# Performance work log

Measured on AMD Instinct MI355X. Metric: run time of the kernel, lower is better.

The kernel has to match this reference:

```python
import jax, jax.numpy as jnp
import numpy as np

B, C, N, K, L = 4, 256, 8192, 4, 3


def _mlp2(h, W1, b1, W2, b2):
    return jax.nn.relu(h @ W1 + b1) @ W2 + b2


def setup_inputs() -> dict:
    key = jax.random.key(0)
    ks = jax.random.split(key, 12)
    s = lambda fan_in: 1.0 / np.sqrt(fan_in)
    inp = {
        "x": jax.random.normal(ks[0], (B, C, N), jnp.float32),
        "points": jax.random.normal(ks[1], (N, 3), jnp.float32),
        "neighbors": jax.random.randint(ks[2], (N, K), 0, N, jnp.int32),
        "edge_W1": jax.random.normal(ks[3], (3, C // 4), jnp.float32) * s(3),
        "edge_b1": jnp.zeros((C // 4,), jnp.float32),
        "edge_W2": jax.random.normal(ks[4], (C // 4, C // 2), jnp.float32) * s(C // 4),
        "edge_b2": jnp.zeros((C // 2,), jnp.float32),
        "msg_W1": jax.random.normal(ks[5], (L, 2 * C + C // 2, 2 * C), jnp.float32) * s(2 * C + C // 2),
        "msg_b1": jnp.zeros((L, 2 * C), jnp.float32),
        "msg_W2": jax.random.normal(ks[6], (L, 2 * C, C), jnp.float32) * s(2 * C),
        "msg_b2": jnp.zeros((L, C), jnp.float32),
        "upd_W1": jax.random.normal(ks[7], (L, 2 * C, 2 * C), jnp.float32) * s(2 * C),
        "upd_b1": jnp.zeros((L, 2 * C), jnp.float32),
        "upd_W2": jax.random.normal(ks[8], (L, 2 * C, C), jnp.float32) * s(2 * C),
        "upd_b2": jnp.zeros((L, C), jnp.float32),
    }
    return inp


def reference(x, points, neighbors, edge_W1, edge_b1, edge_W2, edge_b2,
              msg_W1, msg_b1, msg_W2, msg_b2, upd_W1, upd_b1, upd_W2, upd_b2):
    # x: [B, C, N] -> features [B, N, C]
    feats = jnp.transpose(x, (0, 2, 1))
    # edge features shared across layers: [N, K, C//2]
    edge_vec = points[neighbors] - points[:, None, :]          # [N, K, 3]
    edge_feat = _mlp2(edge_vec, edge_W1, edge_b1, edge_W2, edge_b2)
    for l in range(L):
        sender = feats[:, neighbors, :]                         # [B, N, K, C]
        receiver = jnp.broadcast_to(feats[:, :, None, :], sender.shape)
        ef = jnp.broadcast_to(edge_feat[None], (feats.shape[0],) + edge_feat.shape)
        msg_in = jnp.concatenate([sender, receiver, ef], axis=-1)  # [B,N,K,2.5C]
        msg = _mlp2(msg_in, msg_W1[l], msg_b1[l], msg_W2[l], msg_b2[l])
        agg = jnp.mean(msg, axis=2)                             # [B, N, C]
        upd_in = jnp.concatenate([feats, agg], axis=-1)         # [B, N, 2C]
        feats = _mlp2(upd_in, upd_W1[l], upd_b1[l], upd_W2[l], upd_b2[l])
    return jnp.transpose(feats, (0, 2, 1))
```

## Files before the change

kernel.cpp:

```cpp
#include <hip/hip_runtime.h>

#define DEVI __device__ __forceinline__

typedef unsigned short u16;
typedef unsigned int   u32;
typedef __attribute__((ext_vector_type(8))) short short8;
typedef __attribute__((ext_vector_type(4))) short short4b;
typedef __attribute__((ext_vector_type(4))) float f32x4;

DEVI float bf2f(u16 u) {
    union { u32 i; float f; } x; x.i = ((u32)u) << 16; return x.f;
}
DEVI u16 f2bf(float f) {
    u32 u = __float_as_uint(f);
    u32 r = (u + 0x7FFFu + ((u >> 16) & 1u)) >> 16;
    return (u16)r;
}

DEVI void gload_lds16(const void* g, void* l) {
    __builtin_amdgcn_global_load_lds((const __attribute__((address_space(1))) void*)g,
                                     (__attribute__((address_space(3))) void*)l, 16, 0, 0);
}

struct PJob { u32 dst, soff, tbase, ld, Kd, src; };
__device__ const PJob g_jobs[19] = {
    {0,        0,      0,    128, 64,  4},
    {8192,     0,      8,    512, 256, 0},
    {139264,   131072, 136,  512, 256, 0},
    {270336,   262144, 264,  512, 128, 0},
    {335872,   0,      328,  256, 512, 1},
    {466944,   0,      456,  512, 512, 2},
    {729088,   0,      712,  256, 512, 3},
    {860160,   327680, 840,  512, 256, 0},
    {991232,   458752, 968,  512, 256, 0},
    {1122304,  589824, 1096, 512, 128, 0},
    {1187840,  131072, 1160, 256, 512, 1},
    {1318912,  262144, 1288, 512, 512, 2},
    {1581056,  131072, 1544, 256, 512, 3},
    {1712128,  655360, 1672, 512, 256, 0},
    {1843200,  786432, 1800, 512, 256, 0},
    {1974272,  917504, 1928, 512, 128, 0},
    {2039808,  262144, 1992, 256, 512, 1},
    {2170880,  524288, 2120, 512, 512, 2},
    {2433024,  262144, 2376, 256, 512, 3},
};

__global__ void prep_weights(const float* __restrict__ mW1, const float* __restrict__ mW2,
                             const float* __restrict__ uW1, const float* __restrict__ uW2,
                             const float* __restrict__ eW2, u16* __restrict__ wreg)
{
    int bid = blockIdx.x;
    int ji = 0;
    #pragma unroll
    for (int i = 1; i < 19; ++i) if (bid >= (int)g_jobs[i].tbase) ji = i;
    PJob jb = g_jobs[ji];
    const float* src = (jb.src == 0) ? mW1 : (jb.src == 1) ? mW2 : (jb.src == 2) ? uW1
                     : (jb.src == 3) ? uW2 : eW2;
    src += jb.soff;
    int t  = bid - (int)jb.tbase;
    int nk = (int)jb.Kd >> 5;
    int tk = t % nk, tj = t / nk;
    int k0 = tk * 32, j0 = tj * 32;
    __shared__ float tile[32][33];
    int tx = threadIdx.x, ty = threadIdx.y;
    #pragma unroll
    for (int yy = 0; yy < 4; ++yy) {
        int k = k0 + ty + yy * 8;
        tile[ty + yy * 8][tx] = src[(size_t)k * jb.ld + j0 + tx];
    }
    __syncthreads();
    u16* dst = wreg + jb.dst;
    #pragma unroll
    for (int yy = 0; yy < 4; ++yy) {
        int j = j0 + ty + yy * 8;
        dst[(size_t)j * jb.Kd + k0 + tx] = f2bf(tile[tx][ty + yy * 8]);
    }
}

__global__ __launch_bounds__(256) void conv_w2(const float* __restrict__ mW2,
                                               u16* __restrict__ mW2bf)
{
    int i = blockIdx.x * 256 + threadIdx.x;
    float4 v = *(const float4*)&mW2[(size_t)i * 4];
    short4b o;
    o[0] = (short)f2bf(v.x); o[1] = (short)f2bf(v.y);
    o[2] = (short)f2bf(v.z); o[3] = (short)f2bf(v.w);
    *(short4b*)&mW2bf[(size_t)i * 4] = o;
}

__global__ __launch_bounds__(256) void biasfix(const u16* __restrict__ wreg,
    const float* __restrict__ mb2, const float* __restrict__ ub1,
    float* __restrict__ ub1c)
{
    int idx = blockIdx.x * 256 + threadIdx.x;
    int l = idx >> 9, n = idx & 511;
    const u16* U1T = wreg + 8192 + l * 851968 + 458752;
    const float* b2 = mb2 + l * 256;
    float s = ub1[l * 512 + n];
    for (int j0 = 0; j0 < 256; j0 += 8) {
        short8 wv = *(const short8*)&U1T[(size_t)n * 512 + 256 + j0];
        #pragma unroll
        for (int jj = 0; jj < 8; ++jj) s += bf2f((u16)wv[jj]) * b2[j0 + jj];
    }
    ub1c[idx] = s;
}

__global__ void transpose_in(const float* __restrict__ x, u16* __restrict__ feats)
{
    __shared__ float tile[32][33];
    int n0 = blockIdx.x * 32, c0 = blockIdx.y * 32, b = blockIdx.z;
    int tx = threadIdx.x, ty = threadIdx.y;
    #pragma unroll
    for (int yy = 0; yy < 4; ++yy) {
        int c = c0 + ty + yy * 8;
        tile[ty + yy * 8][tx] = x[((size_t)b * 256 + c) * 8192 + n0 + tx];
    }
    __syncthreads();
    #pragma unroll
    for (int yy = 0; yy < 4; ++yy) {
        int n = n0 + ty + yy * 8;
        feats[((size_t)b * 8192 + n) * 256 + c0 + tx] = f2bf(tile[tx][ty + yy * 8]);
    }
}

__global__ void transpose_out(const u16* __restrict__ feats, float* __restrict__ out)
{
    __shared__ float tile[32][33];
    int n0 = blockIdx.x * 32, c0 = blockIdx.y * 32, b = blockIdx.z;
    int tx = threadIdx.x, ty = threadIdx.y;
    #pragma unroll
    for (int yy = 0; yy < 4; ++yy) {
        int n = n0 + ty + yy * 8;
        tile[ty + yy * 8][tx] = bf2f(feats[((size_t)b * 8192 + n) * 256 + c0 + tx]);
    }
    __syncthreads();
    #pragma unroll
    for (int yy = 0; yy < 4; ++yy) {
        int c = c0 + ty + yy * 8;
        out[((size_t)b * 256 + c) * 8192 + n0 + tx] = tile[tx][ty + yy * 8];
    }
}

__global__ __launch_bounds__(256) void edge_h(
    const float* __restrict__ points, const int* __restrict__ nb,
    const float* __restrict__ W1, const float* __restrict__ b1,
    u16* __restrict__ h)
{
    int e = blockIdx.x * 256 + threadIdx.x;
    int n = e >> 2;
    int j2 = nb[e];
    float p0x = points[n * 3], p0y = points[n * 3 + 1], p0z = points[n * 3 + 2];
    float v0 = points[j2 * 3]     - p0x;
    float v1 = points[j2 * 3 + 1] - p0y;
    float v2 = points[j2 * 3 + 2] - p0z;
    #pragma unroll
    for (int jb = 0; jb < 8; ++jb) {
        short8 o;
        #pragma unroll
        for (int jj = 0; jj < 8; ++jj) {
            int j = jb * 8 + jj;
            float hv = v0 * W1[j] + v1 * W1[64 + j] + v2 * W1[128 + j] + b1[j];
            o[jj] = (short)f2bf(fmaxf(hv, 0.0f));
        }
        *(short8*)&h[(size_t)e * 64 + jb * 8] = o;
    }
}

__global__ __launch_bounds__(256) void gemm_bt(
    const u16* __restrict__ A1, int lda1, int K1,
    const u16* __restrict__ A2, int lda2,
    const u16* __restrict__ B1, int ldb1,
    const u16* __restrict__ B2, int ldb2,
    const float* __restrict__ bias,
    u16* __restrict__ Cp, int ldc,
    int nbn, int Ktot, int relu, int permrows)
{
    __shared__ u16 lds[32768];
    int nwg = (int)gridDim.x;
    int bx0 = (int)blockIdx.x;
    int bx = (bx0 & 7) * (nwg >> 3) + (bx0 >> 3);
    int tn = bx % nbn, tm = bx / nbn;
    int t = threadIdx.x;
    int l = t & 63, w = t >> 6;
    int wrow = (w >> 1) * 64, wcol = (w & 1) * 64;
    int lm = l & 15, lk = l >> 4;
    int swz = lm & 7;
    int rowA = tm * 128;
    int rowB = tn * 128;

    f32x4 acc[4][4];
    #pragma unroll
    for (int mi = 0; mi < 4; ++mi)
        #pragma unroll
        for (int ni = 0; ni < 4; ++ni)
            acc[mi][ni] = (f32x4){0.f, 0.f, 0.f, 0.f};

    auto STAGE = [&](int d, int ks) {
        int kg0 = ks << 6;
        bool useA1 = kg0 < K1;
        const u16* Ab = useA1 ? A1 : A2;
        const u16* Bb = useA1 ? B1 : B2;
        int lda = useA1 ? lda1 : lda2;
        int ldb = useA1 ? ldb1 : ldb2;
        int kg  = useA1 ? kg0 : kg0 - K1;
        u16* At = lds + d * 16384;
        u16* Bt = At + 8192;
        #pragma unroll
        for (int i = 0; i < 4; ++i) {
            int chunk = i * 256 + t;
            int r = chunk >> 3, s = chunk & 7;
            int c = s ^ (r & 7);
            gload_lds16(Ab + (size_t)(rowA + r) * lda + kg + c * 8, &At[chunk * 8]);
        }
        #pragma unroll
        for (int i = 0; i < 4; ++i) {
            int chunk = i * 256 + t;
            int r = chunk >> 3, s = chunk & 7;
            int c = s ^ (r & 7);
            gload_lds16(Bb + (size_t)(rowB + r) * ldb + kg + c * 8, &Bt[chunk * 8]);
        }
    };

    int nks = Ktot >> 6;
    STAGE(0, 0);
    if (nks > 1) STAGE(1, 1);
    int cur = 0;
    for (int ks = 0; ks < nks; ++ks) {
        if (ks + 1 < nks) asm volatile("s_waitcnt vmcnt(8)\n\ts_barrier" ::: "memory");
        else              asm volatile("s_waitcnt vmcnt(0)\n\ts_barrier" ::: "memory");
        const u16* At = lds + cur * 16384;
        const u16* Bt = At + 8192;
        __builtin_amdgcn_s_setprio(1);
        #pragma unroll
        for (int ksub = 0; ksub < 2; ++ksub) {
            int sOff = (((ksub << 2) | lk) ^ swz) << 3;
            short8 af[4], bv[4];
            #pragma unroll
            for (int mi = 0; mi < 4; ++mi)
                af[mi] = *(const short8*)&At[(wrow + mi * 16 + lm) * 64 + sOff];
            #pragma unroll
            for (int ni = 0; ni < 4; ++ni)
                bv[ni] = *(const short8*)&Bt[(wcol + ni * 16 + lm) * 64 + sOff];
            #pragma unroll
            for (int mi = 0; mi < 4; ++mi)
                #pragma unroll
                for (int ni = 0; ni < 4; ++ni)
                    acc[mi][ni] = __builtin_amdgcn_mfma_f32_16x16x32_bf16(af[mi], bv[ni], acc[mi][ni], 0, 0, 0);
        }
        __builtin_amdgcn_s_setprio(0);
        asm volatile("s_barrier" ::: "memory");
        if (ks + 2 < nks) STAGE(cur, ks + 2);
        cur ^= 1;
    }

    #pragma unroll
    for (int ni = 0; ni < 4; ++ni) {
        int col = wcol + ni * 16 + lm;
        float bvl = bias ? bias[tn * 128 + col] : 0.0f;
        #pragma unroll
        for (int mi = 0; mi < 4; ++mi) {
            int row0 = wrow + mi * 16 + lk * 4;
            f32x4 v = acc[mi][ni];
            #pragma unroll
            for (int r = 0; r < 4; ++r) {
                float f = v[r] + bvl;
                if (relu) f = fmaxf(f, 0.0f);
                lds[(row0 + r) * 136 + col] = f2bf(f);
            }
        }
    }
    __syncthreads();
    #pragma unroll
    for (int p = 0; p < 8; ++p) {
        int chunk = p * 256 + t;
        int row = chunk >> 4, sl = chunk & 15;
        short8 v = *(const short8*)&lds[row * 136 + sl * 8];
        int m = tm * 128 + row;
        int orow = permrows ? (((m & 8191) << 2) | (m >> 13)) : m;
        *(short8*)&Cp[(size_t)orow * ldc + tn * 128 + sl * 8] = v;
    }
}

__global__ __launch_bounds__(256) void gather_relu_mean(
    const u16* __restrict__ PR, const u16* __restrict__ E,
    const int* __restrict__ nb, const float* __restrict__ b1,
    u16* __restrict__ hbar)
{
    int b = threadIdx.x >> 6, l = threadIdx.x & 63;
    int c0 = l * 8;
    int n0 = blockIdx.x * 4;

    float4 b1a = *(const float4*)&b1[c0];
    float4 b1b = *(const float4*)&b1[c0 + 4];
    float bb[8] = {b1a.x, b1a.y, b1a.z, b1a.w, b1b.x, b1b.y, b1b.z, b1b.w};

    int4 nbv[4];
    #pragma unroll
    for (int ii = 0; ii < 4; ++ii) nbv[ii] = *(const int4*)&nb[(n0 + ii) * 4];

    #pragma unroll
    for (int ii = 0; ii < 4; ++ii) {
        int n = n0 + ii;
        int nbarr[4] = {nbv[ii].x, nbv[ii].y, nbv[ii].z, nbv[ii].w};

        short8 rv = *(const short8*)&PR[(size_t)(n * 4 + b) * 1024 + 512 + c0];
        float base[8], acc[8];
        #pragma unroll
        for (int j = 0; j < 8; ++j) { base[j] = bf2f((u16)rv[j]) + bb[j]; acc[j] = 0.0f; }

        #pragma unroll
        for (int k = 0; k < 4; ++k) {
            short8 pv = *(const short8*)&PR[(size_t)(nbarr[k] * 4 + b) * 1024 + c0];
            short8 ev = *(const short8*)&E[(size_t)(n * 4 + k) * 512 + c0];
            #pragma unroll
            for (int j = 0; j < 8; ++j) {
                float v = bf2f((u16)pv[j]) + bf2f((u16)ev[j]) + base[j];
                acc[j] += fmaxf(v, 0.0f);
            }
        }
        short8 o;
        #pragma unroll
        for (int j = 0; j < 8; ++j) o[j] = (short)f2bf(acc[j] * 0.25f);
        *(short8*)&hbar[((size_t)(b << 13) + n) * 512 + c0] = o;
    }
}

extern "C" void kernel_launch(void* const* d_in, const int* in_sizes, int n_in,
                              void* d_out, int out_size, void* d_ws, size_t ws_size,
                              hipStream_t stream)
{
    const float* x      = (const float*)d_in[0];
    const float* points = (const float*)d_in[1];
    const int*   nb     = (const int*)d_in[2];
    const float* eW1    = (const float*)d_in[3];
    const float* eb1    = (const float*)d_in[4];
    const float* eW2    = (const float*)d_in[5];
    const float* eb2    = (const float*)d_in[6];
    const float* mW1    = (const float*)d_in[7];
    const float* mb1    = (const float*)d_in[8];
    const float* mW2    = (const float*)d_in[9];
    const float* mb2    = (const float*)d_in[10];
    const float* uW1    = (const float*)d_in[11];
    const float* ub1    = (const float*)d_in[12];
    const float* uW2    = (const float*)d_in[13];
    const float* ub2    = (const float*)d_in[14];
    float* out = (float*)d_out;

    char* ws = (char*)d_ws;
    u16* featsA = (u16*)(ws);
    u16* featsB = (u16*)(ws + 16777216);
    u16* ef     = (u16*)(ws + 33554432);
    u16* PR     = (u16*)(ws + 41943040);
    u16* E      = (u16*)(ws + 109051904);
    u16* hbar   = (u16*)(ws + 142606336);
    u16* wreg   = (u16*)(ws + 176160768);
    u16*   mW2bf = (u16*)(ws + 181288960);
    u16*   WcT   = (u16*)(ws + 182075392);
    float* ub1c  = (float*)(ws + 183648256);
    u16* hEdge  = PR;
    u16* H2     = PR;
    u16* agg    = E;

    const bool fused = (ws_size >= 183654400ull);

    prep_weights<<<2504, dim3(32, 8), 0, stream>>>(mW1, mW2, uW1, uW2, eW2, wreg);
    transpose_in<<<dim3(256, 8, 4), dim3(32, 8), 0, stream>>>(x, featsA);
    edge_h<<<128, 256, 0, stream>>>(points, nb, eW1, eb1, hEdge);
    gemm_bt<<<256, 256, 0, stream>>>(hEdge, 64, 64, hEdge, 64,
                                     wreg, 64, wreg, 64, eb2, ef, 128, 1, 64, 0, 0);

    if (fused) {
        conv_w2<<<384, 256, 0, stream>>>(mW2, mW2bf);
        for (int l = 0; l < 3; ++l) {
            const u16* U1T = wreg + 8192 + l * 851968 + 458752;
            gemm_bt<<<16, 256, 0, stream>>>(U1T + 256, 512, 256, U1T, 512,
                                            mW2bf + l * 131072, 256, mW2bf, 256,
                                            nullptr, WcT + l * 262144, 512, 4, 256, 0, 0);
        }
        biasfix<<<6, 256, 0, stream>>>(wreg, mb2, ub1, ub1c);
    }

    const u16* fin = featsA; u16* fout = featsB;
    for (int lyr = 0; lyr < 3; ++lyr) {
        u16* W1abT = wreg + 8192 + lyr * 851968;
        u16* W1cT  = W1abT + 262144;
        u16* W2T   = W1abT + 327680;
        u16* U1T   = W1abT + 458752;
        u16* U2T   = W1abT + 720896;
        const float* b1  = mb1 + lyr * 512;
        const float* b2  = mb2 + lyr * 256;
        const float* u1b = ub1 + lyr * 512;
        const float* u2b = ub2 + lyr * 256;

        gemm_bt<<<2048, 256, 0, stream>>>((const u16*)fin, 256, 256, (const u16*)fin, 256,
                                          W1abT, 256, W1abT, 256,
                                          nullptr, PR, 1024, 8, 256, 0, 1);
        gemm_bt<<<1024, 256, 0, stream>>>(ef, 128, 128, ef, 128,
                                          W1cT, 128, W1cT, 128,
                                          nullptr, E, 512, 4, 128, 0, 0);
        gather_relu_mean<<<2048, 256, 0, stream>>>(PR, E, nb, b1, hbar);

        if (fused) {
            gemm_bt<<<1024, 256, 0, stream>>>((const u16*)fin, 256, 256, hbar, 512,
                                              U1T, 512, WcT + lyr * 262144, 512,
                                              ub1c + lyr * 512, H2, 512, 4, 768, 1, 0);
        } else {
            gemm_bt<<<512, 256, 0, stream>>>(hbar, 512, 512, hbar, 512,
                                             W2T, 512, W2T, 512,
                                             b2, agg, 256, 2, 512, 0, 0);
            gemm_bt<<<1024, 256, 0, stream>>>((const u16*)fin, 256, 256, agg, 256,
                                              U1T, 512, U1T + 256, 512,
                                              u1b, H2, 512, 4, 512, 1, 0);
        }
        gemm_bt<<<512, 256, 0, stream>>>(H2, 512, 512, H2, 512,
                                         U2T, 512, U2T, 512,
                                         u2b, fout, 256, 2, 512, 0, 0);

        const u16* tmp = fin; fin = fout; fout = (u16*)tmp;
    }
    transpose_out<<<dim3(256, 8, 4), dim3(32, 8), 0, stream>>>(fin, out);
}
```

Before: 453.7 us.

## Use 8-wave 512-thread GEMM blocks and batch weight-fold GEMMs via grid y

The bf16 GEMM now runs 512 threads (8 waves) per 128x128 tile, so each wave computes a 64x32 sub-tile with half the accumulators. Global-to-LDS staging, the vmcnt wait count and the epilogue stores are split across the larger block to match. The three per-layer weight-folding GEMMs are merged into one launch that offsets pointers by blockIdx.y strides. The aim is more waves to hide latency and fewer launches, at the cost of more LDS fragment reloads per MFMA and more barrier participants.

```diff
diff --git a/kernel.cpp b/kernel.cpp
--- a/kernel.cpp
+++ b/kernel.cpp
@@ -166,33 +166,40 @@
     }
 }
 
-__global__ __launch_bounds__(256) void gemm_bt(
+__global__ __launch_bounds__(512, 4) void gemm_bt(
     const u16* __restrict__ A1, int lda1, int K1,
     const u16* __restrict__ A2, int lda2,
     const u16* __restrict__ B1, int ldb1,
     const u16* __restrict__ B2, int ldb2,
     const float* __restrict__ bias,
     u16* __restrict__ Cp, int ldc,
-    int nbn, int Ktot, int relu, int permrows)
+    int nbn, int Ktot, int relu, int permrows,
+    long sA, long sB, long sC)
 {
     __shared__ u16 lds[32768];
+    {
+        long by = blockIdx.y;
+        A1 += by * sA; A2 += by * sA;
+        B1 += by * sB; B2 += by * sB;
+        Cp += by * sC;
+    }
     int nwg = (int)gridDim.x;
     int bx0 = (int)blockIdx.x;
     int bx = (bx0 & 7) * (nwg >> 3) + (bx0 >> 3);
     int tn = bx % nbn, tm = bx / nbn;
     int t = threadIdx.x;
     int l = t & 63, w = t >> 6;
-    int wrow = (w >> 1) * 64, wcol = (w & 1) * 64;
+    int wrow = (w >> 2) * 64, wcol = (w & 3) * 32;
     int lm = l & 15, lk = l >> 4;
     int swz = lm & 7;
     int rowA = tm * 128;
     int rowB = tn * 128;
 
-    f32x4 acc[4][4];
+    f32x4 acc[4][2];
     #pragma unroll
     for (int mi = 0; mi < 4; ++mi)
         #pragma unroll
-        for (int ni = 0; ni < 4; ++ni)
+        for (int ni = 0; ni < 2; ++ni)
             acc[mi][ni] = (f32x4){0.f, 0.f, 0.f, 0.f};
 
     auto STAGE = [&](int d, int ks) {
@@ -206,15 +213,15 @@
         u16* At = lds + d * 16384;
         u16* Bt = At + 8192;
         #pragma unroll
-        for (int i = 0; i < 4; ++i) {
-            int chunk = i * 256 + t;
+        for (int i = 0; i < 2; ++i) {
+            int chunk = i * 512 + t;
             int r = chunk >> 3, s = chunk & 7;
             int c = s ^ (r & 7);
             gload_lds16(Ab + (size_t)(rowA + r) * lda + kg + c * 8, &At[chunk * 8]);
         }
         #pragma unroll
-        for (int i = 0; i < 4; ++i) {
-            int chunk = i * 256 + t;
+        for (int i = 0; i < 2; ++i) {
+            int chunk = i * 512 + t;
             int r = chunk >> 3, s = chunk & 7;
             int c = s ^ (r & 7);
             gload_lds16(Bb + (size_t)(rowB + r) * ldb + kg + c * 8, &Bt[chunk * 8]);
@@ -226,7 +233,7 @@
     if (nks > 1) STAGE(1, 1);
     int cur = 0;
     for (int ks = 0; ks < nks; ++ks) {
-        if (ks + 1 < nks) asm volatile("s_waitcnt vmcnt(8)\n\ts_barrier" ::: "memory");
+        if (ks + 1 < nks) asm volatile("s_waitcnt vmcnt(4)\n\ts_barrier" ::: "memory");
         else              asm volatile("s_waitcnt vmcnt(0)\n\ts_barrier" ::: "memory");
         const u16* At = lds + cur * 16384;
         const u16* Bt = At + 8192;
@@ -234,17 +241,17 @@
         #pragma unroll
         for (int ksub = 0; ksub < 2; ++ksub) {
             int sOff = (((ksub << 2) | lk) ^ swz) << 3;
-            short8 af[4], bv[4];
+            short8 af[4], bv[2];
             #pragma unroll
             for (int mi = 0; mi < 4; ++mi)
                 af[mi] = *(const short8*)&At[(wrow + mi * 16 + lm) * 64 + sOff];
             #pragma unroll
-            for (int ni = 0; ni < 4; ++ni)
+            for (int ni = 0; ni < 2; ++ni)
                 bv[ni] = *(const short8*)&Bt[(wcol + ni * 16 + lm) * 64 + sOff];
             #pragma unroll
             for (int mi = 0; mi < 4; ++mi)
                 #pragma unroll
-                for (int ni = 0; ni < 4; ++ni)
+                for (int ni = 0; ni < 2; ++ni)
                     acc[mi][ni] = __builtin_amdgcn_mfma_f32_16x16x32_bf16(af[mi], bv[ni], acc[mi][ni], 0, 0, 0);
         }
         __builtin_amdgcn_s_setprio(0);
@@ -254,7 +261,7 @@
     }
 
     #pragma unroll
-    for (int ni = 0; ni < 4; ++ni) {
+    for (int ni = 0; ni < 2; ++ni) {
         int col = wcol + ni * 16 + lm;
         float bvl = bias ? bias[tn * 128 + col] : 0.0f;
         #pragma unroll
@@ -271,8 +278,8 @@
     }
     __syncthreads();
     #pragma unroll
-    for (int p = 0; p < 8; ++p) {
-        int chunk = p * 256 + t;
+    for (int p = 0; p < 4; ++p) {
+        int chunk = p * 512 + t;
         int row = chunk >> 4, sl = chunk & 15;
         short8 v = *(const short8*)&lds[row * 136 + sl * 8];
         int m = tm * 128 + row;
@@ -366,16 +373,18 @@
     prep_weights<<<2504, dim3(32, 8), 0, stream>>>(mW1, mW2, uW1, uW2, eW2, wreg);
     transpose_in<<<dim3(256, 8, 4), dim3(32, 8), 0, stream>>>(x, featsA);
     edge_h<<<128, 256, 0, stream>>>(points, nb, eW1, eb1, hEdge);
-    gemm_bt<<<256, 256, 0, stream>>>(hEdge, 64, 64, hEdge, 64,
-                                     wreg, 64, wreg, 64, eb2, ef, 128, 1, 64, 0, 0);
+    gemm_bt<<<256, 512, 0, stream>>>(hEdge, 64, 64, hEdge, 64,
+                                     wreg, 64, wreg, 64, eb2, ef, 128, 1, 64, 0, 0,
+                                     0, 0, 0);
 
     if (fused) {
         conv_w2<<<384, 256, 0, stream>>>(mW2, mW2bf);
-        for (int l = 0; l < 3; ++l) {
-            const u16* U1T = wreg + 8192 + l * 851968 + 458752;
-            gemm_bt<<<16, 256, 0, stream>>>(U1T + 256, 512, 256, U1T, 512,
-                                            mW2bf + l * 131072, 256, mW2bf, 256,
-                                            nullptr, WcT + l * 262144, 512, 4, 256, 0, 0);
+        {
+            const u16* U1T0 = wreg + 8192 + 458752;
+            gemm_bt<<<dim3(16, 3), 512, 0, stream>>>(U1T0 + 256, 512, 256, U1T0, 512,
+                                                     mW2bf, 256, mW2bf, 256,
+                                                     nullptr, WcT, 512, 4, 256, 0, 0,
+                                                     851968, 131072, 262144);
         }
         biasfix<<<6, 256, 0, stream>>>(wreg, mb2, ub1, ub1c);
     }
@@ -392,29 +401,30 @@
         const float* u1b = ub1 + lyr * 512;
         const float* u2b = ub2 + lyr * 256;
 
-        gemm_bt<<<2048, 256, 0, stream>>>((const u16*)fin, 256, 256, (const u16*)fin, 256,
+        gemm_bt<<<2048, 512, 0, stream>>>((const u16*)fin, 256, 256, (const u16*)fin, 256,
                                           W1abT, 256, W1abT, 256,
-                                          nullptr, PR, 1024, 8, 256, 0, 1);
-        gemm_bt<<<1024, 256, 0, stream>>>(ef, 128, 128, ef, 128,
+                                          nullptr, PR, 1024, 8, 256, 0, 1, 0, 0, 0);
+        gemm_bt<<<1024, 512, 0, stream>>>(ef, 128, 128, ef, 128,
                                           W1cT, 128, W1cT, 128,
-                                          nullptr, E, 512, 4, 128, 0, 0);
+                                          nullptr, E, 512, 4, 128, 0, 0, 0, 0, 0);
         gather_relu_mean<<<2048, 256, 0, stream>>>(PR, E, nb, b1, hbar);
 
         if (fused) {
-            gemm_bt<<<1024, 256, 0, stream>>>((const u16*)fin, 256, 256, hbar, 512,
+            gemm_bt<<<1024, 512, 0, stream>>>((const u16*)fin, 256, 256, hbar, 512,
                                               U1T, 512, WcT + lyr * 262144, 512,
-                                              ub1c + lyr * 512, H2, 512, 4, 768, 1, 0);
+                                              ub1c + lyr * 512, H2, 512, 4, 768, 1, 0,
+                                              0, 0, 0);
         } else {
-            gemm_bt<<<512, 256, 0, stream>>>(hbar, 512, 512, hbar, 512,
+            gemm_bt<<<512, 512, 0, stream>>>(hbar, 512, 512, hbar, 512,
                                              W2T, 512, W2T, 512,
-                                             b2, agg, 256, 2, 512, 0, 0);
-            gemm_bt<<<1024, 256, 0, stream>>>((const u16*)fin, 256, 256, agg, 256,
+                                             b2, agg, 256, 2, 512, 0, 0, 0, 0, 0);
+            gemm_bt<<<1024, 512, 0, stream>>>((const u16*)fin, 256, 256, agg, 256,
                                               U1T, 512, U1T + 256, 512,
-                                              u1b, H2, 512, 4, 512, 1, 0);
-        }
-        gemm_bt<<<512, 256, 0, stream>>>(H2, 512, 512, H2, 512,
+                                              u1b, H2, 512, 4, 512, 1, 0, 0, 0, 0);
+        }
+        gemm_bt<<<512, 512, 0, stream>>>(H2, 512, 512, H2, 512,
                                          U2T, 512, U2T, 512,
-                                         u2b, fout, 256, 2, 512, 0, 0);
+                                         u2b, fout, 256, 2, 512, 0, 0, 0, 0, 0);
 
         const u16* tmp = fin; fin = fout; fout = (u16*)tmp;
     }
```

New measurement: 434.3 us. -4.3%, faster.
